# Performance work log

Measured on AMD Instinct MI355X. Metric: run time of the kernel, lower is better.

The kernel has to match this reference:

```python
import jax, jax.numpy as jnp
import numpy as np

K = 3      # kernel size
PAD = 1    # padding


def _conv(x, w, b=None):
    y = jax.lax.conv_general_dilated(
        x, w, window_strides=(1, 1), padding=((PAD, PAD), (PAD, PAD)),
        dimension_numbers=('NCHW', 'OIHW', 'NCHW'))
    if b is not None:
        y = y + b[None, :, None, None]
    return y


def _deform_conv2d(x, offset, mask, weight):
    # torchvision deform_conv2d with offset_groups == C (one offset pair per
    # input channel per kernel tap), stride=1, dilation=1, zero padding.
    B, C, H, W = x.shape
    KK = K * K
    off = offset.reshape(B, C, KK, 2, H, W)   # [...,0]=dy, [...,1]=dx
    dy, dx = off[:, :, :, 0], off[:, :, :, 1]
    m = mask.reshape(B, C, KK, H, W)

    ki = (jnp.arange(KK) // K).reshape(1, 1, KK, 1, 1).astype(x.dtype)
    kj = (jnp.arange(KK) % K).reshape(1, 1, KK, 1, 1).astype(x.dtype)
    gy = jnp.arange(H, dtype=x.dtype).reshape(1, 1, 1, H, 1)
    gx = jnp.arange(W, dtype=x.dtype).reshape(1, 1, 1, 1, W)
    py = dy + gy - PAD + ki   # sampling y coords, [B,C,KK,H,W]
    px = dx + gx - PAD + kj   # sampling x coords

    # torchvision: sample is zero unless -1 < p < size
    valid = (py > -1) & (py < H) & (px > -1) & (px < W)
    y0f = jnp.floor(py)
    x0f = jnp.floor(px)
    wy = py - y0f
    wx = px - x0f
    y0 = y0f.astype(jnp.int32)
    x0 = x0f.astype(jnp.int32)
    y1 = y0 + 1
    x1 = x0 + 1

    xf = x.reshape(B, C, H * W)

    def gather(yi, xi):
        inb = (yi >= 0) & (yi < H) & (xi >= 0) & (xi < W)
        yc = jnp.clip(yi, 0, H - 1)
        xc = jnp.clip(xi, 0, W - 1)
        idx = (yc * W + xc).reshape(B, C, -1)
        v = jnp.take_along_axis(xf, idx, axis=2).reshape(yi.shape)
        return jnp.where(inb, v, jnp.zeros((), x.dtype))

    val = ((1 - wy) * (1 - wx) * gather(y0, x0)
           + (1 - wy) * wx * gather(y0, x1)
           + wy * (1 - wx) * gather(y1, x0)
           + wy * wx * gather(y1, x1))
    samp = jnp.where(valid, val, jnp.zeros((), x.dtype)) * m   # [B,C,KK,H,W]

    O = weight.shape[0]
    return jnp.einsum('bckhw,ock->bohw', samp, weight.reshape(O, C, KK))


def setup_inputs() -> dict:
    key = jax.random.key(0)
    k1, k2, k3, k4, k5, k6 = jax.random.split(key, 6)
    B, C, O, H, W = 8, 64, 128, 64, 64
    KK = K * K
    x = jax.random.normal(k1, (B, C, H, W), dtype=jnp.float32)
    # offset conv: 2*C*KK output channels (module inits to 0; use small random
    # weights so the irregular sampling path is exercised)
    w_off = jax.random.normal(k2, (2 * C * KK, C, K, K), dtype=jnp.float32) * 0.05
    b_off = jnp.zeros((2 * C * KK,), dtype=jnp.float32)
    w_mod = jax.random.normal(k3, (C * KK, C, K, K), dtype=jnp.float32) * 0.05
    b_mod = jax.random.normal(k4, (C * KK,), dtype=jnp.float32) * 0.05
    w_conv = jax.random.normal(k5, (O, C, K, K), dtype=jnp.float32) / np.sqrt(C * KK)
    return {"x": x, "w_off": w_off, "b_off": b_off,
            "w_mod": w_mod, "b_mod": b_mod, "w_conv": w_conv}


def reference(x, w_off, b_off, w_mod, b_mod, w_conv):
    H, W = x.shape[2], x.shape[3]
    max_off = max(H, W) / 4.0
    offset = jnp.clip(_conv(x, w_off, b_off), -max_off, max_off)
    mask = _conv(x, w_mod, b_mod)
    return _deform_conv2d(x, offset, mask, w_conv)
```

## Files before the change

kernel.cpp:

```cpp
#include <hip/hip_runtime.h>
#include <cstddef>
#include <cstdint>

#define TCNT 256

namespace {
constexpr int CIN    = 64;
constexpr int COUT   = 128;
constexpr int HDIM   = 64;
constexpr int WDIM   = 64;
constexpr int HW     = HDIM * WDIM;
constexpr int KD     = CIN * 9;
constexpr int NOFF   = 2 * CIN * 9;
constexpr int NTOT   = NOFF + CIN * 9;
constexpr int NBATCH = 8;
constexpr int HXW    = 66;
constexpr int COPAD  = 1792;
constexpr float MAXOFF = 16.0f;

constexpr size_t XT_ELEMS = (size_t)NBATCH * HXW * HXW * 64;
constexpr size_t WP_ELEMS = (size_t)9 * COPAD * 64;
constexpr size_t WC_ELEMS = (size_t)COUT * KD;
constexpr size_t OFF_XFH  = 0;
constexpr size_t OFF_WPH  = XT_ELEMS;
constexpr size_t OFF_WPL  = XT_ELEMS + WP_ELEMS;
constexpr size_t OFF_WCH  = XT_ELEMS + 2 * WP_ELEMS;
constexpr size_t FIXED_BYTES = (XT_ELEMS + 2 * WP_ELEMS + WC_ELEMS) * 2;
}

typedef __attribute__((ext_vector_type(8))) short    s16x8;
typedef __attribute__((ext_vector_type(8))) _Float16 f16x8;
typedef __attribute__((ext_vector_type(4))) float    f32x4;

__device__ __forceinline__ unsigned short f2h(float v) {
  _Float16 h = (_Float16)v;
  return __builtin_bit_cast(unsigned short, h);
}
__device__ __forceinline__ float h2f(unsigned short u) {
  return (float)__builtin_bit_cast(_Float16, u);
}

__global__ __launch_bounds__(TCNT) void prep_x(
    const float* __restrict__ x, unsigned short* __restrict__ xFh)
{
  const int b  = blockIdx.y;
  const int yy = blockIdx.x;
  const int t  = threadIdx.x;
  unsigned short* oh = xFh + ((size_t)(b * HXW + yy)) * HXW * 64;
  if (yy == 0 || yy == HXW - 1) {
    for (int lin = t; lin < HXW * 64; lin += TCNT) oh[lin] = 0;
    return;
  }
  __shared__ float tile[64][65];
  const int y = yy - 1;
  #pragma unroll
  for (int i = 0; i < 4; ++i) {
    const int f = t + TCNT * i;
    const int c = f >> 4, xq = f & 15;
    const float4 v =
        *(const float4*)(x + ((size_t)(b * 64 + c)) * HW + y * WDIM + xq * 4);
    tile[c][xq * 4 + 0] = v.x; tile[c][xq * 4 + 1] = v.y;
    tile[c][xq * 4 + 2] = v.z; tile[c][xq * 4 + 3] = v.w;
  }
  if (t < 128) {
    const int c = t & 63, xe = (t >> 6) ? (HXW - 1) * 64 : 0;
    oh[xe + c] = 0;
  }
  __syncthreads();
  const int xc = t >> 2, cg = (t & 3) * 16;
  s16x8 h0, h1;
  #pragma unroll
  for (int u = 0; u < 8; ++u) h0[u] = (short)f2h(tile[cg + u][xc]);
  #pragma unroll
  for (int u = 0; u < 8; ++u) h1[u] = (short)f2h(tile[cg + 8 + u][xc]);
  *(s16x8*)(oh + (xc + 1) * 64 + cg)     = h0;
  *(s16x8*)(oh + (xc + 1) * 64 + cg + 8) = h1;
}

__global__ __launch_bounds__(TCNT) void prep_w(
    const float* __restrict__ w_off, const float* __restrict__ w_mod,
    unsigned short* __restrict__ wPh, unsigned short* __restrict__ wPl)
{
  const int co = blockIdx.x;
  const int t  = threadIdx.x;
  const float* wrow = (co < NOFF) ? (w_off + (size_t)co * KD)
                    : (co < NTOT) ? (w_mod + (size_t)(co - NOFF) * KD)
                                  : nullptr;
  for (int lin = t; lin < KD; lin += TCNT) {
    const int r = lin >> 6, c = lin & 63;
    const float v = wrow ? wrow[c * 9 + r] : 0.f;
    const unsigned short hb = f2h(v);
    wPh[((size_t)r * COPAD + co) * 64 + c] = hb;
    wPl[((size_t)r * COPAD + co) * 64 + c] = f2h(v - h2f(hb));
  }
}

__global__ __launch_bounds__(TCNT) void prep_wc(
    const float* __restrict__ w_conv, unsigned short* __restrict__ wCh)
{
  const int o = blockIdx.x;
  const int t = threadIdx.x;
  for (int lin = t; lin < KD; lin += TCNT)
    wCh[(size_t)o * KD + lin] = f2h(w_conv[(size_t)o * KD + lin]);
}

struct StBuf { s16x8 ah0, ah1, bh0, bh1, bl0, bl1; };

__global__ __launch_bounds__(TCNT) void dcn_stage1(
    const unsigned short* __restrict__ xFh,
    const unsigned short* __restrict__ wPh, const unsigned short* __restrict__ wPl,
    const float* __restrict__ b_off, const float* __restrict__ b_mod,
    float* __restrict__ ws, int b0, int nb)
{
  __shared__ unsigned short Ah[128][32];
  __shared__ unsigned short Bh[128][32], Bl[128][32];

  const int t      = threadIdx.x;
  const int Mchunk = nb * HW;
  const int p0  = blockIdx.x * 128;
  const int b   = b0 + (p0 >> 12);
  const int h0  = (p0 & (HW - 1)) >> 6;
  const int co0 = blockIdx.y * 128;

  const int s_row = t >> 1;
  const int s_kh  = t & 1;
  const int s_sw  = ((s_row >> 1) & 3) << 3;
  const int a_h   = h0 + (s_row >> 6);
  const int a_w   = s_row & 63;

  const unsigned short* xbh = xFh + (size_t)b * HXW * HXW * 64;

  const int wave = t >> 6, lane = t & 63;
  const int wm = wave >> 1, wn = wave & 1;
  const int lrow = lane & 15;
  const int lkh  = lane >> 4;

  f32x4 acc[4][4];
  #pragma unroll
  for (int m = 0; m < 4; ++m)
    #pragma unroll
    for (int n = 0; n < 4; ++n) acc[m][n] = (f32x4)0.f;

  StBuf bufA, bufB;

#define STAGE_LOAD(BUF, R, KSUB)                                             \
  {                                                                          \
    const int ki = (R) / 3;                                                  \
    const int kj = (R) - 3 * ki;                                             \
    const size_t aoff = ((size_t)((a_h + ki) * HXW + (a_w + kj))) * 64 +     \
                        (KSUB) * 32 + s_kh * 16;                             \
    BUF.ah0 = *(const s16x8*)(xbh + aoff);                                   \
    BUF.ah1 = *(const s16x8*)(xbh + aoff + 8);                               \
    const size_t boff = ((size_t)(R) * COPAD + co0 + s_row) * 64 +           \
                        (KSUB) * 32 + s_kh * 16;                             \
    BUF.bh0 = *(const s16x8*)(wPh + boff);                                   \
    BUF.bh1 = *(const s16x8*)(wPh + boff + 8);                               \
    BUF.bl0 = *(const s16x8*)(wPl + boff);                                   \
    BUF.bl1 = *(const s16x8*)(wPl + boff + 8);                               \
  }

#define STAGE_WRITE(BUF)                                                     \
  {                                                                          \
    const int c0 = (s_kh * 16) ^ s_sw;                                       \
    const int c1 = (s_kh * 16 + 8) ^ s_sw;                                   \
    *(s16x8*)&Ah[s_row][c0] = BUF.ah0;                                       \
    *(s16x8*)&Ah[s_row][c1] = BUF.ah1;                                       \
    *(s16x8*)&Bh[s_row][c0] = BUF.bh0;                                       \
    *(s16x8*)&Bh[s_row][c1] = BUF.bh1;                                       \
    *(s16x8*)&Bl[s_row][c0] = BUF.bl0;                                       \
    *(s16x8*)&Bl[s_row][c1] = BUF.bl1;                                       \
  }

#define MFMA_PHASE()                                                         \
  {                                                                          \
    f16x8 fa[4];                                                             \
    _Pragma("unroll")                                                        \
    for (int m = 0; m < 4; ++m) {                                            \
      const int r   = wm * 64 + m * 16 + lrow;                               \
      const int col = (lkh * 8) ^ (((r >> 1) & 3) << 3);                     \
      fa[m] = *(const f16x8*)&Ah[r][col];                                    \
    }                                                                        \
    _Pragma("unroll")                                                        \
    for (int n = 0; n < 4; ++n) {                                            \
      const int r   = wn * 64 + n * 16 + lrow;                               \
      const int col = (lkh * 8) ^ (((r >> 1) & 3) << 3);                     \
      const f16x8 fbh = *(const f16x8*)&Bh[r][col];                          \
      const f16x8 fbl = *(const f16x8*)&Bl[r][col];                          \
      _Pragma("unroll")                                                      \
      for (int m = 0; m < 4; ++m) {                                          \
        acc[m][n] = __builtin_amdgcn_mfma_f32_16x16x32_f16(fa[m], fbh, acc[m][n], 0, 0, 0); \
        acc[m][n] = __builtin_amdgcn_mfma_f32_16x16x32_f16(fa[m], fbl, acc[m][n], 0, 0, 0); \
      }                                                                      \
    }                                                                        \
  }

  STAGE_LOAD(bufA, 0, 0)
  #pragma unroll 1
  for (int r = 0; r < 9; ++r) {
    STAGE_WRITE(bufA)
    STAGE_LOAD(bufB, r, 1)
    __syncthreads();
    MFMA_PHASE()
    __syncthreads();
    STAGE_WRITE(bufB)
    if (r < 8) STAGE_LOAD(bufA, r + 1, 0)
    __syncthreads();
    MFMA_PHASE()
    __syncthreads();
  }

  const bool isOff = (co0 < NOFF);
  #pragma unroll
  for (int n = 0; n < 4; ++n) {
    const int cog = co0 + wn * 64 + n * 16 + lrow;
    if (cog >= NTOT) continue;
    const float bias = isOff ? b_off[cog] : b_mod[cog - NOFF];
    float* oplane = ws + (size_t)cog * Mchunk;
    #pragma unroll
    for (int m = 0; m < 4; ++m) {
      f32x4 v = acc[m][n];
      float4 o;
      o.x = v[0] + bias; o.y = v[1] + bias; o.z = v[2] + bias; o.w = v[3] + bias;
      if (isOff) {
        o.x = fminf(MAXOFF, fmaxf(-MAXOFF, o.x));
        o.y = fminf(MAXOFF, fmaxf(-MAXOFF, o.y));
        o.z = fminf(MAXOFF, fmaxf(-MAXOFF, o.z));
        o.w = fminf(MAXOFF, fmaxf(-MAXOFF, o.w));
      }
      const int pb = p0 + wm * 64 + m * 16 + lkh * 4;
      *(float4*)(oplane + pb) = o;
    }
  }
#undef STAGE_LOAD
#undef STAGE_WRITE
#undef MFMA_PHASE
}

__global__ __launch_bounds__(TCNT) void dcn_stage2(
    const float* __restrict__ x, const float* __restrict__ planes,
    const unsigned short* __restrict__ wCh,
    float* __restrict__ out, int b0, int nb)
{
  __shared__ unsigned short SH[32][64], SL[32][64];
  __shared__ unsigned short WH[128][64];

  const int t      = threadIdx.x;
  const int Mchunk = nb * HW;
  const int pc0 = blockIdx.x * 32;
  const int b   = b0 + (pc0 >> 12);
  const int h   = (pc0 & (HW - 1)) >> 6;
  const int w0  = pc0 & 63;

  const int tpx = t & 31;
  const int tsg = t >> 5;
  const int a_swz = (tpx & 7) << 3;
  const float* ws_pix = planes + pc0 + tpx;
  const float* xb     = x + (size_t)b * CIN * HW;

  const int wave = t >> 6, lane = t & 63;
  const int lrow = lane & 15, lkh = lane >> 4;
  const int f_swz = (lrow & 7) << 3;

  f32x4 acc[2][2];
  #pragma unroll
  for (int m = 0; m < 2; ++m)
    #pragma unroll
    for (int n = 0; n < 2; ++n) acc[m][n] = (f32x4)0.f;

  #pragma unroll 1
  for (int sc = 0; sc < 9; ++sc) {
    __syncthreads();
    float vals[8];
    #pragma unroll
    for (int j = 0; j < 8; ++j) {
      const int sl = tsg * 8 + j;
      const int s  = sc * 64 + sl;
      const int c  = s / 9;
      const int kk = s - c * 9;
      const int ki = kk / 3;
      const int kj = kk - ki * 3;
      const float dy = ws_pix[(size_t)(2 * s)     * Mchunk];
      const float dx = ws_pix[(size_t)(2 * s + 1) * Mchunk];
      const float m  = ws_pix[(size_t)(NOFF + s)  * Mchunk];
      const float py = dy + (float)(h + ki - 1);
      const float px = dx + (float)(w0 + tpx + kj - 1);
      const bool valid = (py > -1.f) && (py < (float)HDIM) &&
                         (px > -1.f) && (px < (float)WDIM);
      const float y0f = floorf(py), x0f = floorf(px);
      const float wy = py - y0f, wx = px - x0f;
      const int y0 = (int)y0f, x0 = (int)x0f;
      const float* plane = xb + c * HW;
      float v00 = 0.f, v01 = 0.f, v10 = 0.f, v11 = 0.f;
      if ((unsigned)y0 < (unsigned)HDIM) {
        const float* row = plane + (y0 << 6);
        if ((unsigned)x0       < (unsigned)WDIM) v00 = row[x0];
        if ((unsigned)(x0 + 1) < (unsigned)WDIM) v01 = row[x0 + 1];
      }
      if ((unsigned)(y0 + 1) < (unsigned)HDIM) {
        const float* row = plane + ((y0 + 1) << 6);
        if ((unsigned)x0       < (unsigned)WDIM) v10 = row[x0];
        if ((unsigned)(x0 + 1) < (unsigned)WDIM) v11 = row[x0 + 1];
      }
      const float val = (1.f - wy) * ((1.f - wx) * v00 + wx * v01)
                      + wy         * ((1.f - wx) * v10 + wx * v11);
      vals[j] = valid ? val * m : 0.f;
    }
    {
      s16x8 h8, l8;
      #pragma unroll
      for (int u = 0; u < 8; ++u) {
        const unsigned short hb = f2h(vals[u]);
        h8[u] = (short)hb;
        l8[u] = (short)f2h(vals[u] - h2f(hb));
      }
      const int col = (tsg * 8) ^ a_swz;
      *(s16x8*)&SH[tpx][col] = h8;
      *(s16x8*)&SL[tpx][col] = l8;
    }
    #pragma unroll
    for (int i = 0; i < 4; ++i) {
      const int lin  = t + TCNT * i;
      const int row  = lin >> 3;
      const int slot = lin & 7;
      const size_t g = (size_t)row * KD + sc * 64 + slot * 8;
      const int col  = (slot * 8) ^ ((row & 7) << 3);
      *(s16x8*)&WH[row][col] = *(const s16x8*)(wCh + g);
    }
    __syncthreads();
    #pragma unroll
    for (int ks = 0; ks < 2; ++ks) {
      const int kb = ks * 32 + lkh * 8;
      f16x8 fah[2], fal[2];
      #pragma unroll
      for (int m = 0; m < 2; ++m) {
        const int r   = m * 16 + lrow;
        const int col = kb ^ f_swz;
        fah[m] = *(const f16x8*)&SH[r][col];
        fal[m] = *(const f16x8*)&SL[r][col];
      }
      #pragma unroll
      for (int n = 0; n < 2; ++n) {
        const int r   = wave * 32 + n * 16 + lrow;
        const int col = kb ^ f_swz;
        const f16x8 fbh = *(const f16x8*)&WH[r][col];
        #pragma unroll
        for (int m = 0; m < 2; ++m) {
          acc[m][n] = __builtin_amdgcn_mfma_f32_16x16x32_f16(fah[m], fbh, acc[m][n], 0, 0, 0);
          acc[m][n] = __builtin_amdgcn_mfma_f32_16x16x32_f16(fal[m], fbh, acc[m][n], 0, 0, 0);
        }
      }
    }
  }

  #pragma unroll
  for (int n = 0; n < 2; ++n) {
    const int o = wave * 32 + n * 16 + lrow;
    float* obase = out + ((size_t)(b * COUT + o)) * HW + h * WDIM + w0;
    #pragma unroll
    for (int m = 0; m < 2; ++m) {
      const int pxl = m * 16 + lkh * 4;
      f32x4 v = acc[m][n];
      *(float4*)(obase + pxl) = make_float4(v[0], v[1], v[2], v[3]);
    }
  }
}

extern "C" void kernel_launch(void* const* d_in, const int* in_sizes, int n_in,
                              void* d_out, int out_size, void* d_ws, size_t ws_size,
                              hipStream_t stream) {
  (void)in_sizes; (void)n_in; (void)out_size;
  const float* x      = (const float*)d_in[0];
  const float* w_off  = (const float*)d_in[1];
  const float* b_off  = (const float*)d_in[2];
  const float* w_mod  = (const float*)d_in[3];
  const float* b_mod  = (const float*)d_in[4];
  const float* w_conv = (const float*)d_in[5];
  float* out = (float*)d_out;

  unsigned short* wsu = (unsigned short*)d_ws;
  unsigned short* xFh = wsu + OFF_XFH;
  unsigned short* wPh = wsu + OFF_WPH;
  unsigned short* wPl = wsu + OFF_WPL;
  unsigned short* wCh = wsu + OFF_WCH;
  float* planes = (float*)((char*)d_ws + FIXED_BYTES);

  const size_t ws_per_batch = (size_t)NTOT * HW * sizeof(float);
  size_t avail = (ws_size > FIXED_BYTES) ? (ws_size - FIXED_BYTES) : 0;
  int nb = (int)(avail / ws_per_batch);
  if (nb < 1) nb = 1;
  if (nb > NBATCH) nb = NBATCH;

  prep_x<<<dim3(HXW, NBATCH), TCNT, 0, stream>>>(x, xFh);
  prep_w<<<COPAD, TCNT, 0, stream>>>(w_off, w_mod, wPh, wPl);
  prep_wc<<<COUT, TCNT, 0, stream>>>(w_conv, wCh);

  for (int b0 = 0; b0 < NBATCH; b0 += nb) {
    const int cur = (NBATCH - b0 < nb) ? (NBATCH - b0) : nb;
    dim3 g1(cur * 32, 14);
    dcn_stage1<<<g1, TCNT, 0, stream>>>(xFh, wPh, wPl, b_off, b_mod,
                                        planes, b0, cur);
    dcn_stage2<<<cur * 128, TCNT, 0, stream>>>(x, planes, wCh, out, b0, cur);
  }
}
```

Before: 327.0 us.

## Pre-swizzle weights into MFMA fragment layout and double-buffer LDS in both stages

After: 333.9 us. 2.1% more time.

```diff
diff --git a/kernel.cpp b/kernel.cpp
--- a/kernel.cpp
+++ b/kernel.cpp
@@ -16,11 +16,12 @@
 constexpr int NBATCH = 8;
 constexpr int HXW    = 66;
 constexpr int COPAD  = 1792;
+constexpr int NGT    = COPAD / 16;
 constexpr float MAXOFF = 16.0f;
 
 constexpr size_t XT_ELEMS = (size_t)NBATCH * HXW * HXW * 64;
-constexpr size_t WP_ELEMS = (size_t)9 * COPAD * 64;
-constexpr size_t WC_ELEMS = (size_t)COUT * KD;
+constexpr size_t WP_ELEMS = (size_t)18 * NGT * 512;
+constexpr size_t WC_ELEMS = (size_t)18 * 8 * 512;
 constexpr size_t OFF_XFH  = 0;
 constexpr size_t OFF_WPH  = XT_ELEMS;
 constexpr size_t OFF_WPL  = XT_ELEMS + WP_ELEMS;
@@ -79,41 +80,53 @@
 
 __global__ __launch_bounds__(TCNT) void prep_w(
     const float* __restrict__ w_off, const float* __restrict__ w_mod,
-    unsigned short* __restrict__ wPh, unsigned short* __restrict__ wPl)
+    unsigned short* __restrict__ wF1h, unsigned short* __restrict__ wF1l)
 {
-  const int co = blockIdx.x;
+  const int g  = blockIdx.x;
+  const int hh = blockIdx.y;
+  const int r  = hh >> 1, ks = hh & 1;
   const int t  = threadIdx.x;
-  const float* wrow = (co < NOFF) ? (w_off + (size_t)co * KD)
-                    : (co < NTOT) ? (w_mod + (size_t)(co - NOFF) * KD)
-                                  : nullptr;
-  for (int lin = t; lin < KD; lin += TCNT) {
-    const int r = lin >> 6, c = lin & 63;
-    const float v = wrow ? wrow[c * 9 + r] : 0.f;
+  const size_t base = ((size_t)hh * NGT + g) * 512;
+  #pragma unroll
+  for (int q = 0; q < 2; ++q) {
+    const int e = t + q * 256;
+    const int l = e >> 3, f = e & 7;
+    const int co = g * 16 + (l & 15);
+    const int c  = ks * 32 + (l >> 4) * 8 + f;
+    float v = 0.f;
+    if (co < NOFF)      v = w_off[(size_t)co * KD + c * 9 + r];
+    else if (co < NTOT) v = w_mod[(size_t)(co - NOFF) * KD + c * 9 + r];
     const unsigned short hb = f2h(v);
-    wPh[((size_t)r * COPAD + co) * 64 + c] = hb;
-    wPl[((size_t)r * COPAD + co) * 64 + c] = f2h(v - h2f(hb));
+    wF1h[base + e] = hb;
+    wF1l[base + e] = f2h(v - h2f(hb));
   }
 }
 
 __global__ __launch_bounds__(TCNT) void prep_wc(
-    const float* __restrict__ w_conv, unsigned short* __restrict__ wCh)
+    const float* __restrict__ w_conv, unsigned short* __restrict__ wF2)
 {
-  const int o = blockIdx.x;
-  const int t = threadIdx.x;
-  for (int lin = t; lin < KD; lin += TCNT)
-    wCh[(size_t)o * KD + lin] = f2h(w_conv[(size_t)o * KD + lin]);
-}
-
-struct StBuf { s16x8 ah0, ah1, bh0, bh1, bl0, bl1; };
-
-__global__ __launch_bounds__(TCNT) void dcn_stage1(
+  const int nt = blockIdx.x;
+  const int hh = blockIdx.y;
+  const int sc = hh >> 1, ks = hh & 1;
+  const int t  = threadIdx.x;
+  const size_t base = ((size_t)hh * 8 + nt) * 512;
+  #pragma unroll
+  for (int q = 0; q < 2; ++q) {
+    const int e = t + q * 256;
+    const int l = e >> 3, f = e & 7;
+    const int o = nt * 16 + (l & 15);
+    const int c = sc * 64 + ks * 32 + (l >> 4) * 8 + f;
+    wF2[base + e] = f2h(w_conv[(size_t)o * KD + c]);
+  }
+}
+
+__global__ __launch_bounds__(TCNT, 3) void dcn_stage1(
     const unsigned short* __restrict__ xFh,
-    const unsigned short* __restrict__ wPh, const unsigned short* __restrict__ wPl,
+    const unsigned short* __restrict__ wF1h, const unsigned short* __restrict__ wF1l,
     const float* __restrict__ b_off, const float* __restrict__ b_mod,
     float* __restrict__ ws, int b0, int nb)
 {
-  __shared__ unsigned short Ah[128][32];
-  __shared__ unsigned short Bh[128][32], Bl[128][32];
+  __shared__ unsigned short Ah[2][128][32];
 
   const int t      = threadIdx.x;
   const int Mchunk = nb * HW;
@@ -127,13 +140,13 @@
   const int s_sw  = ((s_row >> 1) & 3) << 3;
   const int a_h   = h0 + (s_row >> 6);
   const int a_w   = s_row & 63;
-
   const unsigned short* xbh = xFh + (size_t)b * HXW * HXW * 64;
 
   const int wave = t >> 6, lane = t & 63;
   const int wm = wave >> 1, wn = wave & 1;
   const int lrow = lane & 15;
   const int lkh  = lane >> 4;
+  const int gbase = (co0 >> 4) + wn * 4;
 
   f32x4 acc[4][4];
   #pragma unroll
@@ -141,73 +154,78 @@
     #pragma unroll
     for (int n = 0; n < 4; ++n) acc[m][n] = (f32x4)0.f;
 
-  StBuf bufA, bufB;
-
-#define STAGE_LOAD(BUF, R, KSUB)                                             \
-  {                                                                          \
-    const int ki = (R) / 3;                                                  \
-    const int kj = (R) - 3 * ki;                                             \
-    const size_t aoff = ((size_t)((a_h + ki) * HXW + (a_w + kj))) * 64 +     \
-                        (KSUB) * 32 + s_kh * 16;                             \
-    BUF.ah0 = *(const s16x8*)(xbh + aoff);                                   \
-    BUF.ah1 = *(const s16x8*)(xbh + aoff + 8);                               \
-    const size_t boff = ((size_t)(R) * COPAD + co0 + s_row) * 64 +           \
-                        (KSUB) * 32 + s_kh * 16;                             \
-    BUF.bh0 = *(const s16x8*)(wPh + boff);                                   \
-    BUF.bh1 = *(const s16x8*)(wPh + boff + 8);                               \
-    BUF.bl0 = *(const s16x8*)(wPl + boff);                                   \
-    BUF.bl1 = *(const s16x8*)(wPl + boff + 8);                               \
-  }
-
-#define STAGE_WRITE(BUF)                                                     \
-  {                                                                          \
-    const int c0 = (s_kh * 16) ^ s_sw;                                       \
-    const int c1 = (s_kh * 16 + 8) ^ s_sw;                                   \
-    *(s16x8*)&Ah[s_row][c0] = BUF.ah0;                                       \
-    *(s16x8*)&Ah[s_row][c1] = BUF.ah1;                                       \
-    *(s16x8*)&Bh[s_row][c0] = BUF.bh0;                                       \
-    *(s16x8*)&Bh[s_row][c1] = BUF.bh1;                                       \
-    *(s16x8*)&Bl[s_row][c0] = BUF.bl0;                                       \
-    *(s16x8*)&Bl[s_row][c1] = BUF.bl1;                                       \
-  }
-
-#define MFMA_PHASE()                                                         \
+  s16x8 rE0, rE1, rO0, rO1;
+  f16x8 wh[4], wl[4];
+
+#define ALOAD(D0, D1, H)                                                     \
+  {                                                                          \
+    const int r_  = (H) >> 1;                                                \
+    const int ks_ = (H) & 1;                                                 \
+    const int ki_ = r_ / 3;                                                  \
+    const int kj_ = r_ - 3 * ki_;                                            \
+    const size_t aoff_ = ((size_t)((a_h + ki_) * HXW + (a_w + kj_))) * 64 +  \
+                         ks_ * 32 + s_kh * 16;                               \
+    D0 = *(const s16x8*)(xbh + aoff_);                                       \
+    D1 = *(const s16x8*)(xbh + aoff_ + 8);                                   \
+  }
+
+#define AWRITE(S0, S1, SEL)                                                  \
+  {                                                                          \
+    const int c0_ = (s_kh * 16) ^ s_sw;                                      \
+    const int c1_ = (s_kh * 16 + 8) ^ s_sw;                                  \
+    *(s16x8*)&Ah[SEL][s_row][c0_] = S0;                                      \
+    *(s16x8*)&Ah[SEL][s_row][c1_] = S1;                                      \
+  }
+
+#define WLOAD(H)                                                             \
+  {                                                                          \
+    _Pragma("unroll")                                                        \
+    for (int n = 0; n < 4; ++n) {                                            \
+      const size_t o_ = ((size_t)(H) * NGT + gbase + n) * 512 + lane * 8;    \
+      wh[n] = *(const f16x8*)(wF1h + o_);                                    \
+      wl[n] = *(const f16x8*)(wF1l + o_);                                    \
+    }                                                                        \
+  }
+
+#define MFMA_P(SEL)                                                          \
   {                                                                          \
     f16x8 fa[4];                                                             \
     _Pragma("unroll")                                                        \
     for (int m = 0; m < 4; ++m) {                                            \
-      const int r   = wm * 64 + m * 16 + lrow;                               \
-      const int col = (lkh * 8) ^ (((r >> 1) & 3) << 3);                     \
-      fa[m] = *(const f16x8*)&Ah[r][col];                                    \
+      const int row = wm * 64 + m * 16 + lrow;                               \
+      const int col = (lkh * 8) ^ (((row >> 1) & 3) << 3);                   \
+      fa[m] = *(const f16x8*)&Ah[SEL][row][col];                             \
     }                                                                        \
     _Pragma("unroll")                                                        \
     for (int n = 0; n < 4; ++n) {                                            \
-      const int r   = wn * 64 + n * 16 + lrow;                               \
-      const int col = (lkh * 8) ^ (((r >> 1) & 3) << 3);                     \
-      const f16x8 fbh = *(const f16x8*)&Bh[r][col];                          \
-      const f16x8 fbl = *(const f16x8*)&Bl[r][col];                          \
       _Pragma("unroll")                                                      \
       for (int m = 0; m < 4; ++m) {                                          \
-        acc[m][n] = __builtin_amdgcn_mfma_f32_16x16x32_f16(fa[m], fbh, acc[m][n], 0, 0, 0); \
-        acc[m][n] = __builtin_amdgcn_mfma_f32_16x16x32_f16(fa[m], fbl, acc[m][n], 0, 0, 0); \
-      }                                                                      \
-    }                                                                        \
-  }
-
-  STAGE_LOAD(bufA, 0, 0)
+        acc[m][n] = __builtin_amdgcn_mfma_f32_16x16x32_f16(fa[m], wh[n], acc[m][n], 0, 0, 0); \
+        acc[m][n] = __builtin_amdgcn_mfma_f32_16x16x32_f16(fa[m], wl[n], acc[m][n], 0, 0, 0); \
+      }                                                                      \
+    }                                                                        \
+  }
+
+  ALOAD(rE0, rE1, 0)
+  WLOAD(0)
+  AWRITE(rE0, rE1, 0)
+  ALOAD(rO0, rO1, 1)
+  __syncthreads();
+
   #pragma unroll 1
-  for (int r = 0; r < 9; ++r) {
-    STAGE_WRITE(bufA)
-    STAGE_LOAD(bufB, r, 1)
+  for (int h = 0; h < 17; ++h) {
+    MFMA_P(h & 1)
+    WLOAD(h + 1)
+    if ((h & 1) == 0) {
+      AWRITE(rO0, rO1, 1)
+      if (h < 16) ALOAD(rE0, rE1, h + 2)
+    } else {
+      AWRITE(rE0, rE1, 0)
+      if (h < 16) ALOAD(rO0, rO1, h + 2)
+    }
     __syncthreads();
-    MFMA_PHASE()
-    __syncthreads();
-    STAGE_WRITE(bufB)
-    if (r < 8) STAGE_LOAD(bufA, r + 1, 0)
-    __syncthreads();
-    MFMA_PHASE()
-    __syncthreads();
-  }
+  }
+  MFMA_P(1)
 
   const bool isOff = (co0 < NOFF);
   #pragma unroll
@@ -231,18 +249,18 @@
       *(float4*)(oplane + pb) = o;
     }
   }
-#undef STAGE_LOAD
-#undef STAGE_WRITE
-#undef MFMA_PHASE
-}
-
-__global__ __launch_bounds__(TCNT) void dcn_stage2(
+#undef ALOAD
+#undef AWRITE
+#undef WLOAD
+#undef MFMA_P
+}
+
+__global__ __launch_bounds__(TCNT, 4) void dcn_stage2(
     const float* __restrict__ x, const float* __restrict__ planes,
-    const unsigned short* __restrict__ wCh,
+    const unsigned short* __restrict__ wF2,
     float* __restrict__ out, int b0, int nb)
 {
-  __shared__ unsigned short SH[32][64], SL[32][64];
-  __shared__ unsigned short WH[128][64];
+  __shared__ unsigned short SH[2][32][64], SL[2][32][64];
 
   const int t      = threadIdx.x;
   const int Mchunk = nb * HW;
@@ -267,90 +285,109 @@
     #pragma unroll
     for (int n = 0; n < 2; ++n) acc[m][n] = (f32x4)0.f;
 
+  float vals[8];
+  f16x8 w4[4];
+
+#define SAMPLE(SCC)                                                          \
+  {                                                                          \
+    _Pragma("unroll")                                                        \
+    for (int j = 0; j < 8; ++j) {                                            \
+      const int sl = tsg * 8 + j;                                            \
+      const int s  = (SCC) * 64 + sl;                                        \
+      const int c  = s / 9;                                                  \
+      const int kk = s - c * 9;                                              \
+      const int ki = kk / 3;                                                 \
+      const int kj = kk - ki * 3;                                            \
+      const float dy = ws_pix[(size_t)(2 * s)     * Mchunk];                 \
+      const float dx = ws_pix[(size_t)(2 * s + 1) * Mchunk];                 \
+      const float m  = ws_pix[(size_t)(NOFF + s)  * Mchunk];                 \
+      const float py = dy + (float)(h + ki - 1);                             \
+      const float px = dx + (float)(w0 + tpx + kj - 1);                      \
+      const bool valid = (py > -1.f) && (py < (float)HDIM) &&                \
+                         (px > -1.f) && (px < (float)WDIM);                  \
+      const float y0f = floorf(py), x0f = floorf(px);                        \
+      const float wy = py - y0f, wx = px - x0f;                              \
+      const int y0 = (int)y0f, x0 = (int)x0f;                                \
+      const float* plane = xb + c * HW;                                      \
+      float v00 = 0.f, v01 = 0.f, v10 = 0.f, v11 = 0.f;                      \
+      if ((unsigned)y0 < (unsigned)HDIM) {                                   \
+        const float* row = plane + (y0 << 6);                                \
+        if ((unsigned)x0       < (unsigned)WDIM) v00 = row[x0];              \
+        if ((unsigned)(x0 + 1) < (unsigned)WDIM) v01 = row[x0 + 1];          \
+      }                                                                      \
+      if ((unsigned)(y0 + 1) < (unsigned)HDIM) {                             \
+        const float* row = plane + ((y0 + 1) << 6);                          \
+        if ((unsigned)x0       < (unsigned)WDIM) v10 = row[x0];              \
+        if ((unsigned)(x0 + 1) < (unsigned)WDIM) v11 = row[x0 + 1];          \
+      }                                                                      \
+      const float val = (1.f - wy) * ((1.f - wx) * v00 + wx * v01)           \
+                      + wy         * ((1.f - wx) * v10 + wx * v11);          \
+      vals[j] = valid ? val * m : 0.f;                                       \
+    }                                                                        \
+  }
+
+#define PACK(SEL)                                                            \
+  {                                                                          \
+    s16x8 h8, l8;                                                            \
+    _Pragma("unroll")                                                        \
+    for (int u = 0; u < 8; ++u) {                                            \
+      const unsigned short hb = f2h(vals[u]);                                \
+      h8[u] = (short)hb;                                                     \
+      l8[u] = (short)f2h(vals[u] - h2f(hb));                                 \
+    }                                                                        \
+    const int col = (tsg * 8) ^ a_swz;                                       \
+    *(s16x8*)&SH[SEL][tpx][col] = h8;                                        \
+    *(s16x8*)&SL[SEL][tpx][col] = l8;                                        \
+  }
+
+#define W2LOAD(SCC)                                                          \
+  {                                                                          \
+    _Pragma("unroll")                                                        \
+    for (int ks = 0; ks < 2; ++ks)                                           \
+      _Pragma("unroll")                                                      \
+      for (int n = 0; n < 2; ++n) {                                          \
+        const size_t o_ = (((size_t)(SCC) * 2 + ks) * 8 + wave * 2 + n) * 512\
+                          + lane * 8;                                        \
+        w4[ks * 2 + n] = *(const f16x8*)(wF2 + o_);                          \
+      }                                                                      \
+  }
+
+#define MFMA2(SEL)                                                           \
+  {                                                                          \
+    _Pragma("unroll")                                                        \
+    for (int ks = 0; ks < 2; ++ks) {                                         \
+      const int colb = (ks * 32 + lkh * 8) ^ f_swz;                          \
+      f16x8 fah[2], fal[2];                                                  \
+      _Pragma("unroll")                                                      \
+      for (int m = 0; m < 2; ++m) {                                          \
+        fah[m] = *(const f16x8*)&SH[SEL][m * 16 + lrow][colb];               \
+        fal[m] = *(const f16x8*)&SL[SEL][m * 16 + lrow][colb];               \
+      }                                                                      \
+      _Pragma("unroll")                                                      \
+      for (int n = 0; n < 2; ++n) {                                          \
+        _Pragma("unroll")                                                    \
+        for (int m = 0; m < 2; ++m) {                                        \
+          acc[m][n] = __builtin_amdgcn_mfma_f32_16x16x32_f16(fah[m], w4[ks * 2 + n], acc[m][n], 0, 0, 0); \
+          acc[m][n] = __builtin_amdgcn_mfma_f32_16x16x32_f16(fal[m], w4[ks * 2 + n], acc[m][n], 0, 0, 0); \
+        }                                                                    \
+      }                                                                      \
+    }                                                                        \
+  }
+
+  SAMPLE(0)
+  PACK(0)
+  W2LOAD(0)
+  __syncthreads();
+
   #pragma unroll 1
-  for (int sc = 0; sc < 9; ++sc) {
+  for (int sc = 0; sc < 8; ++sc) {
+    MFMA2(sc & 1)
+    W2LOAD(sc + 1)
+    SAMPLE(sc + 1)
+    PACK((sc + 1) & 1)
     __syncthreads();
-    float vals[8];
-    #pragma unroll
-    for (int j = 0; j < 8; ++j) {
-      const int sl = tsg * 8 + j;
-      const int s  = sc * 64 + sl;
-      const int c  = s / 9;
-      const int kk = s - c * 9;
-      const int ki = kk / 3;
-      const int kj = kk - ki * 3;
-      const float dy = ws_pix[(size_t)(2 * s)     * Mchunk];
-      const float dx = ws_pix[(size_t)(2 * s + 1) * Mchunk];
-      const float m  = ws_pix[(size_t)(NOFF + s)  * Mchunk];
-      const float py = dy + (float)(h + ki - 1);
-      const float px = dx + (float)(w0 + tpx + kj - 1);
-      const bool valid = (py > -1.f) && (py < (float)HDIM) &&
-                         (px > -1.f) && (px < (float)WDIM);
-      const float y0f = floorf(py), x0f = floorf(px);
-      const float wy = py - y0f, wx = px - x0f;
-      const int y0 = (int)y0f, x0 = (int)x0f;
-      const float* plane = xb + c * HW;
-      float v00 = 0.f, v01 = 0.f, v10 = 0.f, v11 = 0.f;
-      if ((unsigned)y0 < (unsigned)HDIM) {
-        const float* row = plane + (y0 << 6);
-        if ((unsigned)x0       < (unsigned)WDIM) v00 = row[x0];
-        if ((unsigned)(x0 + 1) < (unsigned)WDIM) v01 = row[x0 + 1];
-      }
-      if ((unsigned)(y0 + 1) < (unsigned)HDIM) {
-        const float* row = plane + ((y0 + 1) << 6);
-        if ((unsigned)x0       < (unsigned)WDIM) v10 = row[x0];
-        if ((unsigned)(x0 + 1) < (unsigned)WDIM) v11 = row[x0 + 1];
-      }
-      const float val = (1.f - wy) * ((1.f - wx) * v00 + wx * v01)
-                      + wy         * ((1.f - wx) * v10 + wx * v11);
-      vals[j] = valid ? val * m : 0.f;
-    }
-    {
-      s16x8 h8, l8;
-      #pragma unroll
-      for (int u = 0; u < 8; ++u) {
-        const unsigned short hb = f2h(vals[u]);
-        h8[u] = (short)hb;
-        l8[u] = (short)f2h(vals[u] - h2f(hb));
-      }
-      const int col = (tsg * 8) ^ a_swz;
-      *(s16x8*)&SH[tpx][col] = h8;
-      *(s16x8*)&SL[tpx][col] = l8;
-    }
-    #pragma unroll
-    for (int i = 0; i < 4; ++i) {
-      const int lin  = t + TCNT * i;
-      const int row  = lin >> 3;
-      const int slot = lin & 7;
-      const size_t g = (size_t)row * KD + sc * 64 + slot * 8;
-      const int col  = (slot * 8) ^ ((row & 7) << 3);
-      *(s16x8*)&WH[row][col] = *(const s16x8*)(wCh + g);
-    }
-    __syncthreads();
-    #pragma unroll
-    for (int ks = 0; ks < 2; ++ks) {
-      const int kb = ks * 32 + lkh * 8;
-      f16x8 fah[2], fal[2];
-      #pragma unroll
-      for (int m = 0; m < 2; ++m) {
-        const int r   = m * 16 + lrow;
-        const int col = kb ^ f_swz;
-        fah[m] = *(const f16x8*)&SH[r][col];
-        fal[m] = *(const f16x8*)&SL[r][col];
-      }
-      #pragma unroll
-      for (int n = 0; n < 2; ++n) {
-        const int r   = wave * 32 + n * 16 + lrow;
-        const int col = kb ^ f_swz;
-        const f16x8 fbh = *(const f16x8*)&WH[r][col];
-        #pragma unroll
-        for (int m = 0; m < 2; ++m) {
-          acc[m][n] = __builtin_amdgcn_mfma_f32_16x16x32_f16(fah[m], fbh, acc[m][n], 0, 0, 0);
-          acc[m][n] = __builtin_amdgcn_mfma_f32_16x16x32_f16(fal[m], fbh, acc[m][n], 0, 0, 0);
-        }
-      }
-    }
-  }
+  }
+  MFMA2(0)
 
   #pragma unroll
   for (int n = 0; n < 2; ++n) {
@@ -363,6 +400,10 @@
       *(float4*)(obase + pxl) = make_float4(v[0], v[1], v[2], v[3]);
     }
   }
+#undef SAMPLE
+#undef PACK
+#undef W2LOAD
+#undef MFMA2
 }
 
 extern "C" void kernel_launch(void* const* d_in, const int* in_sizes, int n_in,
@@ -378,10 +419,10 @@
   float* out = (float*)d_out;
 
   unsigned short* wsu = (unsigned short*)d_ws;
-  unsigned short* xFh = wsu + OFF_XFH;
-  unsigned short* wPh = wsu + OFF_WPH;
-  unsigned short* wPl = wsu + OFF_WPL;
-  unsigned short* wCh = wsu + OFF_WCH;
+  unsigned short* xFh  = wsu + OFF_XFH;
+  unsigned short* wF1h = wsu + OFF_WPH;
+  unsigned short* wF1l = wsu + OFF_WPL;
+  unsigned short* wF2  = wsu + OFF_WCH;
   float* planes = (float*)((char*)d_ws + FIXED_BYTES);
 
   const size_t ws_per_batch = (size_t)NTOT * HW * sizeof(float);
@@ -391,14 +432,14 @@
   if (nb > NBATCH) nb = NBATCH;
 
   prep_x<<<dim3(HXW, NBATCH), TCNT, 0, stream>>>(x, xFh);
-  prep_w<<<COPAD, TCNT, 0, stream>>>(w_off, w_mod, wPh, wPl);
-  prep_wc<<<COUT, TCNT, 0, stream>>>(w_conv, wCh);
+  prep_w<<<dim3(NGT, 18), TCNT, 0, stream>>>(w_off, w_mod, wF1h, wF1l);
+  prep_wc<<<dim3(8, 18), TCNT, 0, stream>>>(w_conv, wF2);
 
   for (int b0 = 0; b0 < NBATCH; b0 += nb) {
     const int cur = (NBATCH - b0 < nb) ? (NBATCH - b0) : nb;
     dim3 g1(cur * 32, 14);
-    dcn_stage1<<<g1, TCNT, 0, stream>>>(xFh, wPh, wPl, b_off, b_mod,
+    dcn_stage1<<<g1, TCNT, 0, stream>>>(xFh, wF1h, wF1l, b_off, b_mod,
                                         planes, b0, cur);
-    dcn_stage2<<<cur * 128, TCNT, 0, stream>>>(x, planes, wCh, out, b0, cur);
-  }
-}
+    dcn_stage2<<<cur * 128, TCNT, 0, stream>>>(x, planes, wF2, out, b0, cur);
+  }
+}
```
